# Kernel tuning notes

Measured on AMD Instinct MI355X. Metric: run time of the kernel, lower is better.

## Reference

```python
import jax, jax.numpy as jnp
import numpy as np

NUM_CLASSES = 21
THRESHOLD = 0.5
NEGPOS_RATIO = 3
VAR0, VAR1 = 0.1, 0.2


def setup_inputs() -> dict:
    B, P, T, C = 32, 32768, 64, NUM_CLASSES
    ks = jax.random.split(jax.random.key(0), 7)
    loc_pred = jax.random.normal(ks[0], (B, P, 4), jnp.float32) * 0.1
    conf_pred = jax.random.normal(ks[1], (B, P, C), jnp.float32)
    # priors in center-size form (cx, cy, w, h), all inside unit image
    cxcy = jax.random.uniform(ks[2], (P, 2), jnp.float32, 0.05, 0.95)
    wh = jax.random.uniform(ks[3], (P, 2), jnp.float32, 0.05, 0.3)
    priors = jnp.concatenate([cxcy, wh], axis=1)
    # ground-truth boxes in point form (x1, y1, x2, y2)
    xy1 = jax.random.uniform(ks[4], (B, T, 2), jnp.float32, 0.0, 0.7)
    twh = jax.random.uniform(ks[5], (B, T, 2), jnp.float32, 0.05, 0.3)
    target_boxes = jnp.concatenate([xy1, xy1 + twh], axis=2)
    labels = jax.random.randint(ks[6], (B, T), 1, C, jnp.int32)  # 0 = background
    return {"loc_pred": loc_pred, "conf_pred": conf_pred, "priors": priors,
            "target_boxes": target_boxes, "labels": labels}


def _jaccard(a, b):
    # a: [T,4] point form truths, b: [P,4] point form priors -> [T,P] IoU
    lt = jnp.maximum(a[:, None, :2], b[None, :, :2])
    rb = jnp.minimum(a[:, None, 2:], b[None, :, 2:])
    wh = jnp.clip(rb - lt, 0.0)
    inter = wh[..., 0] * wh[..., 1]
    area_a = ((a[:, 2] - a[:, 0]) * (a[:, 3] - a[:, 1]))[:, None]
    area_b = ((b[:, 2] - b[:, 0]) * (b[:, 3] - b[:, 1]))[None, :]
    return inter / (area_a + area_b - inter)


def _match(truths, labels, priors):
    # truths [T,4] point form, labels [T], priors [P,4] center-size form
    T = truths.shape[0]
    priors_pt = jnp.concatenate([priors[:, :2] - priors[:, 2:] * 0.5,
                                 priors[:, :2] + priors[:, 2:] * 0.5], axis=1)
    iou = _jaccard(truths, priors_pt)                      # [T, P]
    best_prior_idx = jnp.argmax(iou, axis=1)               # [T] best prior per truth
    best_truth_ovr = jnp.max(iou, axis=0)                  # [P]
    best_truth_idx = jnp.argmax(iou, axis=0)               # [P] best truth per prior
    # force-match: every truth keeps its best prior
    best_truth_ovr = best_truth_ovr.at[best_prior_idx].set(2.0)
    best_truth_idx = best_truth_idx.at[best_prior_idx].set(jnp.arange(T))
    matched = truths[best_truth_idx]                       # [P,4] point form
    conf = jnp.where(best_truth_ovr < THRESHOLD, 0, labels[best_truth_idx])
    # encode offsets with variances (SSD)
    g_cxcy = ((matched[:, :2] + matched[:, 2:]) * 0.5 - priors[:, :2]) / (VAR0 * priors[:, 2:])
    g_wh = jnp.log((matched[:, 2:] - matched[:, :2]) / priors[:, 2:]) / VAR1
    return jnp.concatenate([g_cxcy, g_wh], axis=1), conf


def reference(loc_pred, conf_pred, priors, target_boxes, labels):
    B, P, C = conf_pred.shape
    loc_t, conf_t = jax.vmap(lambda t, l: _match(t, l, priors))(target_boxes, labels)
    is_pos = conf_t > 0                                    # [B, P]
    # masked smooth-L1 localization loss (sum over positives)
    diff = jnp.abs(loc_pred - loc_t)
    sl1 = jnp.where(diff < 1.0, 0.5 * diff * diff, diff - 0.5)
    loss_loc = jnp.sum(sl1 * is_pos[..., None].astype(loc_pred.dtype))
    # per-prior cross entropy
    logp = jax.nn.log_softmax(conf_pred, axis=-1)
    ce = -jnp.take_along_axis(logp, conf_t[..., None], axis=-1)[..., 0]  # [B, P]
    # hard negative mining via double argsort (rank of each prior's neg loss)
    neg_conf = jnp.where(is_pos, 0.0, ce)
    loss_idx = jnp.argsort(-neg_conf, axis=1)              # descending
    idx_rank = jnp.argsort(loss_idx, axis=1)
    num_pos = jnp.sum(is_pos.astype(jnp.int32), axis=1, keepdims=True)
    num_neg = jnp.minimum(NEGPOS_RATIO * num_pos, P - 1)
    is_neg = idx_rank < num_neg
    loss_conf = jnp.sum(jnp.where(is_pos | is_neg, ce, 0.0))
    N = jnp.sum(num_pos).astype(loc_pred.dtype)
    return loss_loc / N, loss_conf / N
```

## Files before the change

kernel.cpp:

```cpp
#include <hip/hip_runtime.h>

#define NPRI 32768
#define NT 64
#define NB 32
#define NCLS 21
#define NCHUNK 32
#define NLB 64
#define TBITS 0x3F000000u

__device__ __forceinline__ float smoothl1(float d){
  float a = fabsf(d);
  return a < 1.0f ? 0.5f*a*a : a - 0.5f;
}

__global__ __launch_bounds__(256)
void k_match_ce(const float4* __restrict__ priors, const float4* __restrict__ tboxes,
                const float* __restrict__ conf, unsigned* __restrict__ bestt,
                unsigned* __restrict__ bptc, float* __restrict__ negconf){
  const int chunk = blockIdx.x, b = blockIdx.y, tid = threadIdx.x;
  __shared__ float4 tb[NT];
  __shared__ float tarea[NT];
  __shared__ unsigned tile[16][257];
  if (tid < NT){
    float4 t4 = tboxes[b*NT + tid];
    tb[tid] = t4;
    tarea[tid] = (t4.z - t4.x) * (t4.w - t4.y);
  }
  __syncthreads();
  const int p0 = chunk*1024 + tid;
  float px1_0,py1_0,px2_0,py2_0,pa_0, px1_1,py1_1,px2_1,py2_1,pa_1;
  float px1_2,py1_2,px2_2,py2_2,pa_2, px1_3,py1_3,px2_3,py2_3,pa_3;
#define SETUP(k) { float4 pr = priors[p0 + 256*k]; \
    float hx = pr.z*0.5f, hy = pr.w*0.5f; \
    px1_##k = pr.x-hx; py1_##k = pr.y-hy; px2_##k = pr.x+hx; py2_##k = pr.y+hy; \
    pa_##k = pr.z*pr.w; }
  SETUP(0) SETUP(1) SETUP(2) SETUP(3)
#undef SETUP
  const unsigned inv_0 = 1023u - (unsigned)tid;
  const unsigned inv_1 = 767u  - (unsigned)tid;
  const unsigned inv_2 = 511u  - (unsigned)tid;
  const unsigned inv_3 = 255u  - (unsigned)tid;
  unsigned bp_0 = 0u, bp_1 = 0u, bp_2 = 0u, bp_3 = 0u;
  for (int g = 0; g < 4; ++g){
    #pragma unroll 4
    for (int t16 = 0; t16 < 16; ++t16){
      const int t = g*16 + t16;
      const float4 t4 = tb[t];
      const float ta = tarea[t];
      unsigned q0, q1, q2, q3;
#define IOU(k) { \
      float w = fminf(t4.z,px2_##k) - fmaxf(t4.x,px1_##k); \
      float h = fminf(t4.w,py2_##k) - fmaxf(t4.y,py1_##k); \
      w = fmaxf(w,0.f); h = fmaxf(h,0.f); \
      float inter = w*h; \
      float iou = inter * __builtin_amdgcn_rcpf(ta + pa_##k - inter); \
      unsigned ib = __float_as_uint(iou); \
      unsigned pk = (ib & 0xFFFFFFC0u) | (unsigned)(63 - t); \
      if (pk > bp_##k) bp_##k = pk; \
      q##k = (ib & 0xFFFFFC00u) | inv_##k; }
      IOU(0) IOU(1) IOU(2) IOU(3)
#undef IOU
      unsigned m01 = q0 > q1 ? q0 : q1;
      unsigned m23 = q2 > q3 ? q2 : q3;
      tile[t16][tid] = m01 > m23 ? m01 : m23;
    }
    __syncthreads();
    {
      const int r = tid >> 4, j = tid & 15;
      unsigned mx = 0u;
      #pragma unroll
      for (int i = 0; i < 16; ++i){
        unsigned v = tile[r][j*16 + i];
        mx = mx > v ? mx : v;
      }
      #pragma unroll
      for (int off = 1; off < 16; off <<= 1){
        unsigned o = (unsigned)__shfl_xor((int)mx, off);
        mx = mx > o ? mx : o;
      }
      if (j == 0)
        bptc[((size_t)b*NT + g*16 + r)*NCHUNK + chunk] = mx;
    }
    __syncthreads();
  }
  const size_t ob = (size_t)b*NPRI + p0;
  bestt[ob]       = bp_0;
  bestt[ob + 256] = bp_1;
  bestt[ob + 512] = bp_2;
  bestt[ob + 768] = bp_3;
  const int pc = chunk*1024 + tid*4;
  const float4* g4 = (const float4*)(conf + ((size_t)b*NPRI + pc)*NCLS);
  float s0=0.f,s1=0.f,s2=0.f,s3=0.f, x00=0.f,x01=0.f,x02=0.f,x03=0.f;
  #pragma unroll
  for (int j = 0; j < 21; ++j){
    float4 v = g4[j];
    #pragma unroll
    for (int c = 0; c < 4; ++c){
      const int idx = 4*j + c;
      const float f = (c==0) ? v.x : (c==1) ? v.y : (c==2) ? v.z : v.w;
      const float e = __expf(f);
      if (idx < 21)      { s0 += e; if (idx == 0)  x00 = f; }
      else if (idx < 42) { s1 += e; if (idx == 21) x01 = f; }
      else if (idx < 63) { s2 += e; if (idx == 42) x02 = f; }
      else               { s3 += e; if (idx == 63) x03 = f; }
    }
  }
  float4 o;
  o.x = __logf(s0) - x00;
  o.y = __logf(s1) - x01;
  o.z = __logf(s2) - x02;
  o.w = __logf(s3) - x03;
  *(float4*)(negconf + (size_t)b*NPRI + pc) = o;
}

__global__ __launch_bounds__(256)
void k_loss(const float4* __restrict__ priors, const float4* __restrict__ tboxes,
            const int* __restrict__ labels, const float* __restrict__ conf,
            const float4* __restrict__ loc, const unsigned* __restrict__ bestt,
            const unsigned* __restrict__ bptc, float* __restrict__ negconf,
            float* __restrict__ part_loc, float* __restrict__ part_ce,
            int* __restrict__ part_cnt){
  const int b = blockIdx.y, tid = threadIdx.x;
  const int base = blockIdx.x * 512;
  __shared__ float4 tb[NT];
  __shared__ int slab[NT];
  __shared__ int fm[512];
  fm[tid] = -1; fm[tid + 256] = -1;
  if (tid < NT){
    tb[tid] = tboxes[b*NT + tid];
    slab[tid] = labels[b*NT + tid];
  }
  __syncthreads();
  if (tid < NT){
    const unsigned* src = bptc + ((size_t)b*NT + tid)*NCHUNK;
    unsigned kk = 0u; int bc = 0;
    #pragma unroll
    for (int c = 0; c < NCHUNK; ++c){
      unsigned v = src[c];
      if (v > kk){ kk = v; bc = c; }
    }
    const int p = bc*1024 + 1023 - (int)(kk & 1023u);
    unsigned d = (unsigned)(p - base);
    if (d < 512u) atomicMax(&fm[d], tid);
  }
  __syncthreads();
  float lloc = 0.f, posce = 0.f;
  int cnt = 0;
  #pragma unroll
  for (int k = 0; k < 2; ++k){
    const int sl = tid + 256*k;
    const int p = base + sl;
    const size_t idx = (size_t)b*NPRI + p;
    const unsigned bt = bestt[idx];
    const int f = fm[sl];
    if ((f >= 0) || (bt >= TBITS)){
      const int t = (f >= 0) ? f : (63 - (int)(bt & 63u));
      float4 pr = priors[p];
      float4 t4 = tb[t];
      float4 lp = loc[idx];
      float gcx = ((t4.x+t4.z)*0.5f - pr.x) / (0.1f*pr.z);
      float gcy = ((t4.y+t4.w)*0.5f - pr.y) / (0.1f*pr.w);
      float gw = __logf((t4.z-t4.x)/pr.z) * 5.f;
      float gh = __logf((t4.w-t4.y)/pr.w) * 5.f;
      lloc += smoothl1(lp.x-gcx)+smoothl1(lp.y-gcy)+smoothl1(lp.z-gw)+smoothl1(lp.w-gh);
      const int cls = slab[t];
      posce += negconf[idx] + conf[idx*NCLS] - conf[idx*NCLS + cls];
      negconf[idx] = 0.f;
      cnt++;
    }
  }
  for (int off = 32; off; off >>= 1){
    lloc  += __shfl_xor(lloc, off);
    posce += __shfl_xor(posce, off);
    cnt   += __shfl_xor(cnt, off);
  }
  __shared__ float r0[4], r1[4];
  __shared__ int r2[4];
  if ((tid & 63) == 0){ int w = tid>>6; r0[w]=lloc; r1[w]=posce; r2[w]=cnt; }
  __syncthreads();
  if (tid == 0){
    float a0=0.f, a1=0.f; int c=0;
    #pragma unroll
    for (int w = 0; w < 4; ++w){ a0+=r0[w]; a1+=r1[w]; c+=r2[w]; }
    const int o = b*NLB + blockIdx.x;
    part_loc[o] = a0;
    part_ce[o]  = a1;
    part_cnt[o] = c;
  }
}

__global__ __launch_bounds__(1024)
void k_mine(const float* __restrict__ negconf, const int* __restrict__ part_cnt,
            float* __restrict__ part_mine){
  const int b = blockIdx.x, tid = threadIdx.x;
  __shared__ int sk;
  if (tid < NLB){
    int c = part_cnt[b*NLB + tid];
    for (int off = 32; off; off >>= 1) c += __shfl_xor(c, off);
    if (tid == 0) sk = min(3*c, NPRI-1);
  }
  __syncthreads();
  const int k = sk;
  if (k <= 0){ if (tid == 0) part_mine[b] = 0.f; return; }
  const float* nc = negconf + (size_t)b*NPRI;
  unsigned v[32];
  #pragma unroll
  for (int i = 0; i < 32; ++i) v[i] = __float_as_uint(nc[tid + i*1024]);
  __shared__ int scnt[2][16];
  unsigned cur = 0u;
  for (int bit = 30; bit >= 0; --bit){
    const unsigned cand = cur | (1u << bit);
    int c = 0;
    #pragma unroll
    for (int i = 0; i < 32; ++i)
      c += (int)__popcll(__ballot(v[i] >= cand));
    if ((tid & 63) == 0) scnt[bit & 1][tid>>6] = c;
    __syncthreads();
    int tot = 0;
    #pragma unroll
    for (int w = 0; w < 16; ++w) tot += scnt[bit & 1][w];
    if (tot >= k) cur = cand;
  }
  float sgt = 0.f; int cgt = 0;
  #pragma unroll
  for (int i = 0; i < 32; ++i){
    if (v[i] > cur){ sgt += __uint_as_float(v[i]); cgt++; }
  }
  for (int off = 32; off; off >>= 1){
    sgt += __shfl_xor(sgt, off);
    cgt += __shfl_xor(cgt, off);
  }
  __shared__ float ss[16];
  __shared__ int sc[16];
  if ((tid & 63) == 0){ ss[tid>>6] = sgt; sc[tid>>6] = cgt; }
  __syncthreads();
  if (tid == 0){
    float st = 0.f; int ct = 0;
    #pragma unroll
    for (int w = 0; w < 16; ++w){ st += ss[w]; ct += sc[w]; }
    part_mine[b] = st + (float)(k - ct) * __uint_as_float(cur);
  }
}

__global__ __launch_bounds__(1024)
void k_final(const float* __restrict__ part_loc, const float* __restrict__ part_ce,
             const int* __restrict__ part_cnt, const float* __restrict__ part_mine,
             float* __restrict__ out){
  const int tid = threadIdx.x;
  float sl = 0.f, se = 0.f; int sc_ = 0;
  #pragma unroll
  for (int i = tid; i < NB*NLB; i += 1024){
    sl += part_loc[i];
    se += part_ce[i];
    sc_ += part_cnt[i];
  }
  float sm = (tid < NB) ? part_mine[tid] : 0.f;
  for (int off = 32; off; off >>= 1){
    sl += __shfl_xor(sl, off);
    se += __shfl_xor(se, off);
    sm += __shfl_xor(sm, off);
    sc_ += __shfl_xor(sc_, off);
  }
  __shared__ float a0[16], a1[16], a2[16];
  __shared__ int a3[16];
  if ((tid & 63) == 0){ int w = tid>>6; a0[w]=sl; a1[w]=se; a2[w]=sm; a3[w]=sc_; }
  __syncthreads();
  if (tid == 0){
    float t0=0.f, t1=0.f, t2=0.f; int n=0;
    #pragma unroll
    for (int w = 0; w < 16; ++w){ t0+=a0[w]; t1+=a1[w]; t2+=a2[w]; n+=a3[w]; }
    float N = (float)n;
    out[0] = t0 / N;
    out[1] = (t1 + t2) / N;
  }
}

extern "C" void kernel_launch(void* const* d_in, const int* in_sizes, int n_in,
                              void* d_out, int out_size, void* d_ws, size_t ws_size,
                              hipStream_t stream){
  (void)in_sizes; (void)n_in; (void)out_size; (void)ws_size;
  const float4* loc    = (const float4*)d_in[0];
  const float*  conf   = (const float*) d_in[1];
  const float4* priors = (const float4*)d_in[2];
  const float4* tboxes = (const float4*)d_in[3];
  const int*    labels = (const int*)   d_in[4];
  float* out = (float*)d_out;

  char* ws = (char*)d_ws;
  size_t off = 0;
  float* negconf = (float*)(ws + off);            off += (size_t)NB*NPRI*4;
  unsigned* bestt = (unsigned*)(ws + off);        off += (size_t)NB*NPRI*4;
  unsigned* bptc = (unsigned*)(ws + off);         off += (size_t)NB*NT*NCHUNK*4;
  float* part_loc = (float*)(ws + off);           off += (size_t)NB*NLB*4;
  float* part_ce  = (float*)(ws + off);           off += (size_t)NB*NLB*4;
  int*   part_cnt = (int*)(ws + off);             off += (size_t)NB*NLB*4;
  float* part_mine = (float*)(ws + off);          off += NB*4;

  k_match_ce<<<dim3(NCHUNK, NB), 256, 0, stream>>>(priors, tboxes, conf,
                                                   bestt, bptc, negconf);
  k_loss <<<dim3(NLB, NB), 256, 0, stream>>>(priors, tboxes, labels, conf, loc,
                                             bestt, bptc, negconf,
                                             part_loc, part_ce, part_cnt);
  k_mine <<<NB, 1024, 0, stream>>>(negconf, part_cnt, part_mine);
  k_final<<<1, 1024, 0, stream>>>(part_loc, part_ce, part_cnt, part_mine, out);
}
```

Measured before the change: 90.46 us.

## Interleave conf logit loads with IoU groups and fix tile reduction bank conflicts

Issues the per-prior conf float4 loads in batches before each 16-truth IoU group and consumes them afterwards, so global memory latency is hidden behind the IoU ALU work instead of being exposed at the end. The shared tile read pattern changes from contiguous per-lane segments to a strided interleave, and the row padding goes from 257 to 272, to reduce LDS bank conflicts in the reduction. Holding up to six float4 buffers live across the IoU loop raises register pressure and may lower occupancy.

```diff
diff --git a/kernel.cpp b/kernel.cpp
--- a/kernel.cpp
+++ b/kernel.cpp
@@ -20,7 +20,7 @@
   const int chunk = blockIdx.x, b = blockIdx.y, tid = threadIdx.x;
   __shared__ float4 tb[NT];
   __shared__ float tarea[NT];
-  __shared__ unsigned tile[16][257];
+  __shared__ unsigned tile[16][272];
   if (tid < NT){
     float4 t4 = tboxes[b*NT + tid];
     tb[tid] = t4;
@@ -41,70 +41,81 @@
   const unsigned inv_2 = 511u  - (unsigned)tid;
   const unsigned inv_3 = 255u  - (unsigned)tid;
   unsigned bp_0 = 0u, bp_1 = 0u, bp_2 = 0u, bp_3 = 0u;
-  for (int g = 0; g < 4; ++g){
-    #pragma unroll 4
-    for (int t16 = 0; t16 < 16; ++t16){
-      const int t = g*16 + t16;
-      const float4 t4 = tb[t];
-      const float ta = tarea[t];
-      unsigned q0, q1, q2, q3;
+
+  const int pc = chunk*1024 + tid*4;
+  const float4* g4 = (const float4*)(conf + ((size_t)b*NPRI + pc)*NCLS);
+  float s0=0.f,s1=0.f,s2=0.f,s3=0.f, x00=0.f,x01=0.f,x02=0.f,x03=0.f;
+  float4 cb0,cb1,cb2,cb3,cb4,cb5;
+#define CELL(idx, f) { float e = __expf(f); \
+    if ((idx) < 21)      { s0 += e; if ((idx) == 0)  x00 = f; } \
+    else if ((idx) < 42) { s1 += e; if ((idx) == 21) x01 = f; } \
+    else if ((idx) < 63) { s2 += e; if ((idx) == 42) x02 = f; } \
+    else                 { s3 += e; if ((idx) == 63) x03 = f; } }
+#define CONS(j, B) CELL(4*(j)+0, B.x) CELL(4*(j)+1, B.y) CELL(4*(j)+2, B.z) CELL(4*(j)+3, B.w)
+
+#define GROUP(g) { \
+    _Pragma("unroll 4") \
+    for (int t16 = 0; t16 < 16; ++t16){ \
+      const int t = (g)*16 + t16; \
+      const float4 t4 = tb[t]; \
+      const float ta = tarea[t]; \
+      unsigned q0, q1, q2, q3; \
+      IOU(0) IOU(1) IOU(2) IOU(3) \
+      unsigned m01 = q0 > q1 ? q0 : q1; \
+      unsigned m23 = q2 > q3 ? q2 : q3; \
+      tile[t16][tid] = m01 > m23 ? m01 : m23; \
+    } \
+    __syncthreads(); \
+    { \
+      const int r = tid >> 4, j = tid & 15; \
+      unsigned mx = 0u; \
+      _Pragma("unroll") \
+      for (int i = 0; i < 16; ++i){ \
+        unsigned v = tile[r][i*16 + j]; \
+        mx = mx > v ? mx : v; \
+      } \
+      _Pragma("unroll") \
+      for (int off = 1; off < 16; off <<= 1){ \
+        unsigned o = (unsigned)__shfl_xor((int)mx, off); \
+        mx = mx > o ? mx : o; \
+      } \
+      if (j == 0) \
+        bptc[((size_t)b*NT + (g)*16 + r)*NCHUNK + chunk] = mx; \
+    } \
+    __syncthreads(); }
 #define IOU(k) { \
-      float w = fminf(t4.z,px2_##k) - fmaxf(t4.x,px1_##k); \
-      float h = fminf(t4.w,py2_##k) - fmaxf(t4.y,py1_##k); \
-      w = fmaxf(w,0.f); h = fmaxf(h,0.f); \
-      float inter = w*h; \
-      float iou = inter * __builtin_amdgcn_rcpf(ta + pa_##k - inter); \
-      unsigned ib = __float_as_uint(iou); \
-      unsigned pk = (ib & 0xFFFFFFC0u) | (unsigned)(63 - t); \
-      if (pk > bp_##k) bp_##k = pk; \
-      q##k = (ib & 0xFFFFFC00u) | inv_##k; }
-      IOU(0) IOU(1) IOU(2) IOU(3)
+    float w = fminf(t4.z,px2_##k) - fmaxf(t4.x,px1_##k); \
+    float h = fminf(t4.w,py2_##k) - fmaxf(t4.y,py1_##k); \
+    w = fmaxf(w,0.f); h = fmaxf(h,0.f); \
+    float inter = w*h; \
+    float iou = inter * __builtin_amdgcn_rcpf(ta + pa_##k - inter); \
+    unsigned ib = __float_as_uint(iou); \
+    unsigned pk = (ib & 0xFFFFFFC0u) | (unsigned)(63 - t); \
+    if (pk > bp_##k) bp_##k = pk; \
+    q##k = (ib & 0xFFFFFC00u) | inv_##k; }
+
+  cb0 = g4[0]; cb1 = g4[1]; cb2 = g4[2]; cb3 = g4[3]; cb4 = g4[4];
+  GROUP(0)
+  CONS(0,cb0) CONS(1,cb1) CONS(2,cb2) CONS(3,cb3) CONS(4,cb4)
+  cb0 = g4[5]; cb1 = g4[6]; cb2 = g4[7]; cb3 = g4[8]; cb4 = g4[9];
+  GROUP(1)
+  CONS(5,cb0) CONS(6,cb1) CONS(7,cb2) CONS(8,cb3) CONS(9,cb4)
+  cb0 = g4[10]; cb1 = g4[11]; cb2 = g4[12]; cb3 = g4[13]; cb4 = g4[14];
+  GROUP(2)
+  CONS(10,cb0) CONS(11,cb1) CONS(12,cb2) CONS(13,cb3) CONS(14,cb4)
+  cb0 = g4[15]; cb1 = g4[16]; cb2 = g4[17]; cb3 = g4[18]; cb4 = g4[19]; cb5 = g4[20];
+  GROUP(3)
+  CONS(15,cb0) CONS(16,cb1) CONS(17,cb2) CONS(18,cb3) CONS(19,cb4) CONS(20,cb5)
 #undef IOU
-      unsigned m01 = q0 > q1 ? q0 : q1;
-      unsigned m23 = q2 > q3 ? q2 : q3;
-      tile[t16][tid] = m01 > m23 ? m01 : m23;
-    }
-    __syncthreads();
-    {
-      const int r = tid >> 4, j = tid & 15;
-      unsigned mx = 0u;
-      #pragma unroll
-      for (int i = 0; i < 16; ++i){
-        unsigned v = tile[r][j*16 + i];
-        mx = mx > v ? mx : v;
-      }
-      #pragma unroll
-      for (int off = 1; off < 16; off <<= 1){
-        unsigned o = (unsigned)__shfl_xor((int)mx, off);
-        mx = mx > o ? mx : o;
-      }
-      if (j == 0)
-        bptc[((size_t)b*NT + g*16 + r)*NCHUNK + chunk] = mx;
-    }
-    __syncthreads();
-  }
+#undef GROUP
+#undef CONS
+#undef CELL
+
   const size_t ob = (size_t)b*NPRI + p0;
   bestt[ob]       = bp_0;
   bestt[ob + 256] = bp_1;
   bestt[ob + 512] = bp_2;
   bestt[ob + 768] = bp_3;
-  const int pc = chunk*1024 + tid*4;
-  const float4* g4 = (const float4*)(conf + ((size_t)b*NPRI + pc)*NCLS);
-  float s0=0.f,s1=0.f,s2=0.f,s3=0.f, x00=0.f,x01=0.f,x02=0.f,x03=0.f;
-  #pragma unroll
-  for (int j = 0; j < 21; ++j){
-    float4 v = g4[j];
-    #pragma unroll
-    for (int c = 0; c < 4; ++c){
-      const int idx = 4*j + c;
-      const float f = (c==0) ? v.x : (c==1) ? v.y : (c==2) ? v.z : v.w;
-      const float e = __expf(f);
-      if (idx < 21)      { s0 += e; if (idx == 0)  x00 = f; }
-      else if (idx < 42) { s1 += e; if (idx == 21) x01 = f; }
-      else if (idx < 63) { s2 += e; if (idx == 42) x02 = f; }
-      else               { s3 += e; if (idx == 63) x03 = f; }
-    }
-  }
   float4 o;
   o.x = __logf(s0) - x00;
   o.y = __logf(s1) - x01;
```

After: 86.33 us. -4.6%, faster.
